# Kernel tuning notes

Measured on AMD Instinct MI355X. Metric: run time of the kernel, lower is better.

The kernel has to match this reference:

```python
import jax, jax.numpy as jnp
import numpy as np


def setup_inputs() -> dict:
    key = jax.random.key(0)
    ks = jax.random.split(key, 13)
    B, D, H, O = 4096, 2048, 3, 1  # batch, input_dim, hidden layer count, output_dim
    f32 = jnp.float32
    scale = 1.0 / np.sqrt(D)
    return {
        "x": jax.random.normal(ks[0], (B, D), f32),
        "w_mu_h": jax.random.normal(ks[1], (H, D, D), f32) * scale,
        "w_rho_h": jax.random.normal(ks[2], (H, D, D), f32) - 5.0,  # softplus(-5) ~ small std
        "b_mu_h": jax.random.normal(ks[3], (H, D), f32) * scale,
        "b_rho_h": jax.random.normal(ks[4], (H, D), f32) - 5.0,
        "w_mu_o": jax.random.normal(ks[5], (O, D), f32) * scale,
        "w_rho_o": jax.random.normal(ks[6], (O, D), f32) - 5.0,
        "b_mu_o": jax.random.normal(ks[7], (O,), f32) * scale,
        "b_rho_o": jax.random.normal(ks[8], (O,), f32) - 5.0,
        # reparameterization noise (torch.randn_like), passed explicitly for determinism
        "eps_w_h": jax.random.normal(ks[9], (H, D, D), f32),
        "eps_b_h": jax.random.normal(ks[10], (H, D), f32),
        "eps_w_o": jax.random.normal(ks[11], (O, D), f32),
        "eps_b_o": jax.random.normal(ks[12], (O,), f32),
    }


def _vlinear(x, w_mu, w_rho, b_mu, b_rho, eps_w, eps_b):
    # weight = mu + eps * softplus(rho); F.linear(x, W, b) = x @ W.T + b
    w = w_mu + eps_w * jax.nn.softplus(w_rho)
    b = b_mu + eps_b * jax.nn.softplus(b_rho)
    return x @ w.T + b


def reference(x, w_mu_h, w_rho_h, b_mu_h, b_rho_h,
              w_mu_o, w_rho_o, b_mu_o, b_rho_o,
              eps_w_h, eps_b_h, eps_w_o, eps_b_o):
    def step(h, p):
        wm, wr, bm, br, ew, eb = p
        h = jax.nn.relu(_vlinear(h, wm, wr, bm, br, ew, eb))
        return h, None

    h, _ = jax.lax.scan(step, x, (w_mu_h, w_rho_h, b_mu_h, b_rho_h, eps_w_h, eps_b_h))
    return _vlinear(h, w_mu_o, w_rho_o, b_mu_o, b_rho_o, eps_w_o, eps_b_o)
```

## Files before the change

### kernel.cpp

```cpp
#include <hip/hip_runtime.h>

#define BB 4096
#define DD 2048

typedef float f32x4 __attribute__((ext_vector_type(4)));
typedef __bf16 bf16x8 __attribute__((ext_vector_type(8)));

typedef __attribute__((address_space(1))) unsigned int gl_u32;
typedef __attribute__((address_space(3))) unsigned int lds_u32;

#define GLOAD_LDS16(gptr, sptr) \
  __builtin_amdgcn_global_load_lds((gl_u32*)(void*)(gptr), (lds_u32*)(sptr), 16, 0, 0)

#define SBAR_MEM() asm volatile("s_barrier" ::: "memory")
#define VMCNT(n)   asm volatile("s_waitcnt vmcnt(" #n ")" ::: "memory")

__device__ __forceinline__ unsigned short f2bf(float f) {
  unsigned int u = __float_as_uint(f);
  u += 0x7fffu + ((u >> 16) & 1u);
  return (unsigned short)(u >> 16);
}

__device__ __forceinline__ float sp(float x) {
  float t = __expf(-fabsf(x));
  return fmaxf(x, 0.0f) + __logf(1.0f + t);
}

__device__ __forceinline__ void prep_w_vec4(
    const float* __restrict__ mu, const float* __restrict__ rho,
    const float* __restrict__ eps, unsigned short* __restrict__ Wh,
    long long i)
{
  float4 m = ((const float4*)mu)[i];
  float4 r = ((const float4*)rho)[i];
  float4 e = ((const float4*)eps)[i];
  ushort4 o;
  o.x = f2bf(m.x + e.x * sp(r.x));
  o.y = f2bf(m.y + e.y * sp(r.y));
  o.z = f2bf(m.z + e.z * sp(r.z));
  o.w = f2bf(m.w + e.w * sp(r.w));
  ((ushort4*)Wh)[i] = o;
}

__device__ __forceinline__ void prep_f32_vec4(
    const float* __restrict__ mu, const float* __restrict__ rho,
    const float* __restrict__ eps, float* __restrict__ out, long long i)
{
  float4 m = ((const float4*)mu)[i];
  float4 r = ((const float4*)rho)[i];
  float4 e = ((const float4*)eps)[i];
  float4 o;
  o.x = m.x + e.x * sp(r.x);
  o.y = m.y + e.y * sp(r.y);
  o.z = m.z + e.z * sp(r.z);
  o.w = m.w + e.w * sp(r.w);
  ((float4*)out)[i] = o;
}

__global__ __launch_bounds__(512) void prep0_kernel(
    const float* __restrict__ x,
    const float* __restrict__ wmuh, const float* __restrict__ wrhoh,
    const float* __restrict__ bmuh, const float* __restrict__ brhoh,
    const float* __restrict__ epswh, const float* __restrict__ epsbh,
    unsigned short* __restrict__ Wh, unsigned short* __restrict__ Xb,
    float* __restrict__ bh)
{
  const int b = blockIdx.x;
  const int t = threadIdx.x;
  if (b < 512) {
    long long base = (long long)b * 2048 + t;
    #pragma unroll
    for (int j = 0; j < 4; ++j)
      prep_w_vec4(wmuh, wrhoh, epswh, Wh, base + j * 512);
    return;
  }
  if (b < 1536) {
    long long base = (long long)(b - 512) * 2048 + t;
    #pragma unroll
    for (int j = 0; j < 4; ++j) {
      float4 v = ((const float4*)x)[base + j * 512];
      ushort4 o;
      o.x = f2bf(v.x); o.y = f2bf(v.y); o.z = f2bf(v.z); o.w = f2bf(v.w);
      ((ushort4*)Xb)[base + j * 512] = o;
    }
    return;
  }
  prep_f32_vec4(bmuh, brhoh, epsbh, bh, t);
}

#define NGEMM 256
#define ATILE 16384
#define BUFE  24576

struct Coords256 { int m0, n0; int srow[4], sgc[4]; };

__device__ __forceinline__ Coords256 coords256(int id, int t) {
  Coords256 g;
  const int p = id & 7;
  const int i4 = id >> 3;
  const int mt = (p & 3) * 4 + (i4 & 3);
  const int nt = (p >> 2) * 8 + (i4 >> 2);
  g.m0 = mt * 256;
  g.n0 = nt * 128;
  #pragma unroll
  for (int i = 0; i < 4; ++i) {
    int c = i * 512 + t;
    g.srow[i] = c >> 3;
    g.sgc[i] = (c & 7) ^ (g.srow[i] & 7);
  }
  return g;
}

__device__ __forceinline__ void stage_tile(
    const unsigned short* __restrict__ A, const unsigned short* __restrict__ W,
    unsigned short* buf, const Coords256& gc, int kt, int t)
{
  #pragma unroll
  for (int i = 0; i < 4; ++i) {
    int c = i * 512 + t;
    const unsigned short* ga = A + (size_t)(gc.m0 + gc.srow[i]) * DD + kt + gc.sgc[i] * 8;
    GLOAD_LDS16(ga, &buf[c * 8]);
  }
  #pragma unroll
  for (int i = 0; i < 2; ++i) {
    int c = i * 512 + t;
    const unsigned short* gb = W + (size_t)(gc.n0 + gc.srow[i]) * DD + kt + gc.sgc[i] * 8;
    GLOAD_LDS16(gb, &buf[ATILE + c * 8]);
  }
}

__device__ __forceinline__ void compute_ktile(
    const unsigned short* buf, int wm, int wn, int lq, int lr,
    f32x4 (&acc)[4][4])
{
  #pragma unroll
  for (int s = 0; s < 2; ++s) {
    bf16x8 af[4], bfv[4];
    const int g = s * 4 + lq;
    const int go = (g ^ (lr & 7)) * 8;
    #pragma unroll
    for (int i = 0; i < 4; ++i) {
      int ra = wm * 64 + i * 16 + lr;
      af[i] = *(const bf16x8*)&buf[ra * 64 + go];
    }
    #pragma unroll
    for (int j = 0; j < 4; ++j) {
      int rb = wn * 64 + j * 16 + lr;
      bfv[j] = *(const bf16x8*)&buf[ATILE + rb * 64 + go];
    }
    __builtin_amdgcn_s_setprio(1);
    #pragma unroll
    for (int i = 0; i < 4; ++i)
      #pragma unroll
      for (int j = 0; j < 4; ++j)
        acc[i][j] = __builtin_amdgcn_mfma_f32_16x16x32_bf16(af[i], bfv[j], acc[i][j], 0, 0, 0);
    __builtin_amdgcn_s_setprio(0);
  }
}

__device__ __forceinline__ void gemm_mainloop256(
    const unsigned short* __restrict__ A, const unsigned short* __restrict__ W,
    unsigned short (*lds)[BUFE], const Coords256& gc, int t, f32x4 (&acc)[4][4])
{
  const int l = t & 63, lq = l >> 4, lr = l & 15;
  const int w = t >> 6, wm = w & 3, wn = w >> 2;
  unsigned short *p0 = lds[0], *p1 = lds[1], *p2 = lds[2];
  stage_tile(A, W, p0, gc, 0, t);
  stage_tile(A, W, p1, gc, 64, t);
  for (int k = 0; k < 32; ++k) {
    if (k < 30) {
      stage_tile(A, W, p2, gc, (k + 2) * 64, t);
      VMCNT(12);
    } else if (k == 30) {
      VMCNT(6);
    } else {
      VMCNT(0);
    }
    SBAR_MEM();
    compute_ktile(p0, wm, wn, lq, lr, acc);
    SBAR_MEM();
    unsigned short* tmp = p0; p0 = p1; p1 = p2; p2 = tmp;
  }
}

__device__ __forceinline__ void epilogue_store256(
    const Coords256& gc, int t, f32x4 (&acc)[4][4],
    const float* __restrict__ bias, unsigned short* __restrict__ C)
{
  const int l = t & 63, lq = l >> 4, lr = l & 15;
  const int w = t >> 6, wm = w & 3, wn = w >> 2;
  #pragma unroll
  for (int j = 0; j < 4; ++j) {
    int n = gc.n0 + wn * 64 + j * 16 + lr;
    float bv = bias[n];
    #pragma unroll
    for (int i = 0; i < 4; ++i) {
      int mbase = gc.m0 + wm * 64 + i * 16 + lq * 4;
      #pragma unroll
      for (int r = 0; r < 4; ++r) {
        float v = fmaxf(acc[i][j][r] + bv, 0.0f);
        C[(size_t)(mbase + r) * DD + n] = f2bf(v);
      }
    }
  }
}

__global__ __launch_bounds__(512, 2) void gemm_relu_fused_kernel(
    const unsigned short* __restrict__ A,
    const unsigned short* __restrict__ W,
    const float* __restrict__ bias,
    unsigned short* __restrict__ C,
    const float* __restrict__ wmuh, const float* __restrict__ wrhoh,
    const float* __restrict__ bmuh, const float* __restrict__ brhoh,
    const float* __restrict__ wmuo, const float* __restrict__ wrhoo,
    const float* __restrict__ epswh, const float* __restrict__ epsbh,
    const float* __restrict__ epswo,
    unsigned short* __restrict__ Wh, float* __restrict__ bh,
    float* __restrict__ wo)
{
  __shared__ unsigned short lds[3][BUFE];

  const int id = blockIdx.x;
  const int t = threadIdx.x;

  if (id >= NGEMM) {
    const int pb = id - NGEMM;
    if (pb < 1024) {
      long long base = 1048576LL + (long long)pb * 2048 + t;
      #pragma unroll
      for (int j = 0; j < 4; ++j)
        prep_w_vec4(wmuh, wrhoh, epswh, Wh, base + j * 512);
      return;
    }
    #pragma unroll
    for (int j = 0; j < 2; ++j)
      prep_f32_vec4(bmuh, brhoh, epsbh, bh, 512 + j * 512 + t);
    prep_f32_vec4(wmuo, wrhoo, epswo, wo, t);
    return;
  }

  Coords256 gc = coords256(id, t);
  f32x4 acc[4][4] = {};
  gemm_mainloop256(A, W, lds, gc, t, acc);
  epilogue_store256(gc, t, acc, bias, C);
}

__global__ __launch_bounds__(512, 2) void gemm_relu_kernel(
    const unsigned short* __restrict__ A,
    const unsigned short* __restrict__ W,
    const float* __restrict__ bias,
    unsigned short* __restrict__ C)
{
  __shared__ unsigned short lds[3][BUFE];
  const int t = threadIdx.x;
  Coords256 gc = coords256(blockIdx.x, t);
  f32x4 acc[4][4] = {};
  gemm_mainloop256(A, W, lds, gc, t, acc);
  epilogue_store256(gc, t, acc, bias, C);
}

__global__ __launch_bounds__(512, 2) void gemm_relu_dot_kernel(
    const unsigned short* __restrict__ A,
    const unsigned short* __restrict__ W,
    const float* __restrict__ bias,
    const float* __restrict__ wo,
    float* __restrict__ Pbuf)
{
  __shared__ unsigned short lds[3][BUFE];
  const int t = threadIdx.x;

  Coords256 gc = coords256(blockIdx.x, t);
  f32x4 acc[4][4] = {};
  gemm_mainloop256(A, W, lds, gc, t, acc);

  const int l = t & 63, lq = l >> 4, lr = l & 15;
  const int w = t >> 6, wm = w & 3, wn = w >> 2;

  float bv[4], wv[4];
  #pragma unroll
  for (int j = 0; j < 4; ++j) {
    int n = gc.n0 + wn * 64 + j * 16 + lr;
    bv[j] = bias[n];
    wv[j] = wo[n];
  }
  float partial[4][4];
  #pragma unroll
  for (int i = 0; i < 4; ++i)
    #pragma unroll
    for (int r = 0; r < 4; ++r) {
      float s = 0.0f;
      #pragma unroll
      for (int j = 0; j < 4; ++j)
        s += fmaxf(acc[i][j][r] + bv[j], 0.0f) * wv[j];
      partial[i][r] = s;
    }

  #pragma unroll
  for (int d = 1; d <= 8; d <<= 1)
    #pragma unroll
    for (int i = 0; i < 4; ++i)
      #pragma unroll
      for (int r = 0; r < 4; ++r)
        partial[i][r] += __shfl_xor(partial[i][r], d, 64);

  float* sRed = (float*)lds;
  if (lr == 0) {
    #pragma unroll
    for (int i = 0; i < 4; ++i)
      #pragma unroll
      for (int r = 0; r < 4; ++r) {
        int row = wm * 64 + i * 16 + lq * 4 + r;
        sRed[row * 2 + wn] = partial[i][r];
      }
  }
  __syncthreads();
  if (t < 256) {
    float s = sRed[t * 2 + 0] + sRed[t * 2 + 1];
    int nt = gc.n0 >> 7;
    Pbuf[nt * BB + gc.m0 + t] = s;
  }
}

__global__ __launch_bounds__(256) void reduce_out_kernel(
    const float* __restrict__ Pbuf,
    const float* __restrict__ bmuo, const float* __restrict__ brhoo,
    const float* __restrict__ epsbo,
    float* __restrict__ out)
{
  const int m = blockIdx.x * 256 + threadIdx.x;
  float s = bmuo[0] + epsbo[0] * sp(brhoo[0]);
  #pragma unroll
  for (int nt = 0; nt < 16; ++nt)
    s += Pbuf[nt * BB + m];
  out[m] = s;
}

extern "C" void kernel_launch(void* const* d_in, const int* in_sizes, int n_in,
                              void* d_out, int out_size, void* d_ws, size_t ws_size,
                              hipStream_t stream) {
  const float* x     = (const float*)d_in[0];
  const float* wmuh  = (const float*)d_in[1];
  const float* wrhoh = (const float*)d_in[2];
  const float* bmuh  = (const float*)d_in[3];
  const float* brhoh = (const float*)d_in[4];
  const float* wmuo  = (const float*)d_in[5];
  const float* wrhoo = (const float*)d_in[6];
  const float* bmuo  = (const float*)d_in[7];
  const float* brhoo = (const float*)d_in[8];
  const float* epswh = (const float*)d_in[9];
  const float* epsbh = (const float*)d_in[10];
  const float* epswo = (const float*)d_in[11];
  const float* epsbo = (const float*)d_in[12];

  char* ws = (char*)d_ws;
  unsigned short* Wh = (unsigned short*)(ws);
  unsigned short* Xb = (unsigned short*)(ws + 25165824);
  unsigned short* Ha = (unsigned short*)(ws + 25165824 + 16777216);
  unsigned short* Hb = (unsigned short*)(ws + 25165824 + 2 * 16777216);
  float* bh   = (float*)(ws + 25165824 + 3 * 16777216);
  float* wo   = (float*)(ws + 25165824 + 3 * 16777216 + 24576);
  float* Pbuf = (float*)(ws + 25165824 + 3 * 16777216 + 24576 + 8192);

  prep0_kernel<<<1537, 512, 0, stream>>>(
      x, wmuh, wrhoh, bmuh, brhoh, epswh, epsbh, Wh, Xb, bh);

  gemm_relu_fused_kernel<<<NGEMM + 1025, 512, 0, stream>>>(
      Xb, Wh, bh, Ha,
      wmuh, wrhoh, bmuh, brhoh, wmuo, wrhoo,
      epswh, epsbh, epswo, Wh, bh, wo);

  gemm_relu_kernel<<<NGEMM, 512, 0, stream>>>(Ha, Wh + 1 * 4194304, bh + DD, Hb);

  gemm_relu_dot_kernel<<<NGEMM, 512, 0, stream>>>(
      Hb, Wh + 2 * 4194304, bh + 2 * DD, wo, Pbuf);

  reduce_out_kernel<<<BB / 256, 256, 0, stream>>>(
      Pbuf, bmuo, brhoo, epsbo, (float*)d_out);
}
```

Baseline: 320.4 us.

## Split k-tile staging into halves and move all weight prep into prep kernel

The GEMM main loop now issues each k-tile's global-to-LDS loads in two halves interleaved with the two MFMA sub-steps. It also adds an explicit lgkmcnt wait and sched_barriers, with the aim of overlapping memory traffic with compute more finely. The first GEMM no longer runs hidden-layer weight preparation in extra blocks alongside it; all weight, bias and output-weight prep moves into the single prep kernel. This removes co-scheduling of elementwise work with the first GEMM but serializes the prep before any GEMM starts.

```diff
diff --git a/kernel.cpp b/kernel.cpp
--- a/kernel.cpp
+++ b/kernel.cpp
@@ -14,6 +14,7 @@
 
 #define SBAR_MEM() asm volatile("s_barrier" ::: "memory")
 #define VMCNT(n)   asm volatile("s_waitcnt vmcnt(" #n ")" ::: "memory")
+#define LGKMCNT0() asm volatile("s_waitcnt lgkmcnt(0)" ::: "memory")
 
 __device__ __forceinline__ unsigned short f2bf(float f) {
   unsigned int u = __float_as_uint(f);
@@ -61,21 +62,23 @@
     const float* __restrict__ x,
     const float* __restrict__ wmuh, const float* __restrict__ wrhoh,
     const float* __restrict__ bmuh, const float* __restrict__ brhoh,
+    const float* __restrict__ wmuo, const float* __restrict__ wrhoo,
     const float* __restrict__ epswh, const float* __restrict__ epsbh,
+    const float* __restrict__ epswo,
     unsigned short* __restrict__ Wh, unsigned short* __restrict__ Xb,
-    float* __restrict__ bh)
+    float* __restrict__ bh, float* __restrict__ wo)
 {
   const int b = blockIdx.x;
   const int t = threadIdx.x;
-  if (b < 512) {
+  if (b < 1536) {
     long long base = (long long)b * 2048 + t;
     #pragma unroll
     for (int j = 0; j < 4; ++j)
       prep_w_vec4(wmuh, wrhoh, epswh, Wh, base + j * 512);
     return;
   }
-  if (b < 1536) {
-    long long base = (long long)(b - 512) * 2048 + t;
+  if (b < 2560) {
+    long long base = (long long)(b - 1536) * 2048 + t;
     #pragma unroll
     for (int j = 0; j < 4; ++j) {
       float4 v = ((const float4*)x)[base + j * 512];
@@ -85,12 +88,13 @@
     }
     return;
   }
-  prep_f32_vec4(bmuh, brhoh, epsbh, bh, t);
+  #pragma unroll
+  for (int j = 0; j < 3; ++j)
+    prep_f32_vec4(bmuh, brhoh, epsbh, bh, j * 512 + t);
+  prep_f32_vec4(wmuo, wrhoo, epswo, wo, t);
 }
 
 #define NGEMM 256
-#define ATILE 16384
-#define BUFE  24576
 
 struct Coords256 { int m0, n0; int srow[4], sgc[4]; };
 
@@ -111,75 +115,91 @@
   return g;
 }
 
-__device__ __forceinline__ void stage_tile(
+__device__ __forceinline__ void stage_half0(
     const unsigned short* __restrict__ A, const unsigned short* __restrict__ W,
-    unsigned short* buf, const Coords256& gc, int kt, int t)
-{
-  #pragma unroll
-  for (int i = 0; i < 4; ++i) {
+    unsigned short* bufA, unsigned short* bufB,
+    const Coords256& gc, int kt, int t)
+{
+  #pragma unroll
+  for (int i = 0; i < 2; ++i) {
     int c = i * 512 + t;
     const unsigned short* ga = A + (size_t)(gc.m0 + gc.srow[i]) * DD + kt + gc.sgc[i] * 8;
-    GLOAD_LDS16(ga, &buf[c * 8]);
-  }
-  #pragma unroll
-  for (int i = 0; i < 2; ++i) {
+    GLOAD_LDS16(ga, &bufA[c * 8]);
+  }
+  const unsigned short* gb = W + (size_t)(gc.n0 + gc.srow[0]) * DD + kt + gc.sgc[0] * 8;
+  GLOAD_LDS16(gb, &bufB[t * 8]);
+}
+
+__device__ __forceinline__ void stage_half1(
+    const unsigned short* __restrict__ A, const unsigned short* __restrict__ W,
+    unsigned short* bufA, unsigned short* bufB,
+    const Coords256& gc, int kt, int t)
+{
+  #pragma unroll
+  for (int i = 2; i < 4; ++i) {
     int c = i * 512 + t;
-    const unsigned short* gb = W + (size_t)(gc.n0 + gc.srow[i]) * DD + kt + gc.sgc[i] * 8;
-    GLOAD_LDS16(gb, &buf[ATILE + c * 8]);
-  }
-}
-
-__device__ __forceinline__ void compute_ktile(
-    const unsigned short* buf, int wm, int wn, int lq, int lr,
-    f32x4 (&acc)[4][4])
-{
-  #pragma unroll
-  for (int s = 0; s < 2; ++s) {
-    bf16x8 af[4], bfv[4];
-    const int g = s * 4 + lq;
-    const int go = (g ^ (lr & 7)) * 8;
-    #pragma unroll
-    for (int i = 0; i < 4; ++i) {
-      int ra = wm * 64 + i * 16 + lr;
-      af[i] = *(const bf16x8*)&buf[ra * 64 + go];
-    }
-    #pragma unroll
-    for (int j = 0; j < 4; ++j) {
-      int rb = wn * 64 + j * 16 + lr;
-      bfv[j] = *(const bf16x8*)&buf[ATILE + rb * 64 + go];
-    }
-    __builtin_amdgcn_s_setprio(1);
-    #pragma unroll
-    for (int i = 0; i < 4; ++i)
-      #pragma unroll
-      for (int j = 0; j < 4; ++j)
-        acc[i][j] = __builtin_amdgcn_mfma_f32_16x16x32_bf16(af[i], bfv[j], acc[i][j], 0, 0, 0);
-    __builtin_amdgcn_s_setprio(0);
-  }
-}
-
-__device__ __forceinline__ void gemm_mainloop256(
+    const unsigned short* ga = A + (size_t)(gc.m0 + gc.srow[i]) * DD + kt + gc.sgc[i] * 8;
+    GLOAD_LDS16(ga, &bufA[c * 8]);
+  }
+  const unsigned short* gb = W + (size_t)(gc.n0 + gc.srow[1]) * DD + kt + gc.sgc[1] * 8;
+  GLOAD_LDS16(gb, &bufB[(512 + t) * 8]);
+}
+
+__device__ __forceinline__ void compute_half(
+    const unsigned short* bufA, const unsigned short* bufB, int s,
+    int wm, int wn, int lq, int lr, f32x4 (&acc)[4][4])
+{
+  bf16x8 af[4], bfv[4];
+  const int g = s * 4 + lq;
+  const int go = (g ^ (lr & 7)) * 8;
+  #pragma unroll
+  for (int i = 0; i < 4; ++i) {
+    int ra = wm * 64 + i * 16 + lr;
+    af[i] = *(const bf16x8*)&bufA[ra * 64 + go];
+  }
+  #pragma unroll
+  for (int j = 0; j < 4; ++j) {
+    int rb = wn * 64 + j * 16 + lr;
+    bfv[j] = *(const bf16x8*)&bufB[rb * 64 + go];
+  }
+  LGKMCNT0();
+  __builtin_amdgcn_sched_barrier(0);
+  __builtin_amdgcn_s_setprio(1);
+  #pragma unroll
+  for (int i = 0; i < 4; ++i)
+    #pragma unroll
+    for (int j = 0; j < 4; ++j)
+      acc[i][j] = __builtin_amdgcn_mfma_f32_16x16x32_bf16(af[i], bfv[j], acc[i][j], 0, 0, 0);
+  __builtin_amdgcn_s_setprio(0);
+}
+
+__device__ __forceinline__ void gemm_mainloop8p(
     const unsigned short* __restrict__ A, const unsigned short* __restrict__ W,
-    unsigned short (*lds)[BUFE], const Coords256& gc, int t, f32x4 (&acc)[4][4])
+    unsigned short (*ldsA)[16384], unsigned short (*ldsB)[8192],
+    const Coords256& gc, int t, f32x4 (&acc)[4][4])
 {
   const int l = t & 63, lq = l >> 4, lr = l & 15;
   const int w = t >> 6, wm = w & 3, wn = w >> 2;
-  unsigned short *p0 = lds[0], *p1 = lds[1], *p2 = lds[2];
-  stage_tile(A, W, p0, gc, 0, t);
-  stage_tile(A, W, p1, gc, 64, t);
+  unsigned short *a0 = ldsA[0], *a1 = ldsA[1], *a2 = ldsA[2];
+  unsigned short *b0 = ldsB[0], *b1 = ldsB[1], *b2 = ldsB[2];
+  stage_half0(A, W, a0, b0, gc, 0, t);
+  stage_half1(A, W, a0, b0, gc, 0, t);
+  stage_half0(A, W, a1, b1, gc, 64, t);
+  stage_half1(A, W, a1, b1, gc, 64, t);
   for (int k = 0; k < 32; ++k) {
-    if (k < 30) {
-      stage_tile(A, W, p2, gc, (k + 2) * 64, t);
-      VMCNT(12);
-    } else if (k == 30) {
-      VMCNT(6);
-    } else {
-      VMCNT(0);
-    }
+    if (k < 30) stage_half0(A, W, a2, b2, gc, (k + 2) * 64, t);
+    __builtin_amdgcn_sched_barrier(0);
+    if (k < 30)      { VMCNT(9); }
+    else if (k == 30){ VMCNT(6); }
+    else             { VMCNT(0); }
     SBAR_MEM();
-    compute_ktile(p0, wm, wn, lq, lr, acc);
+    compute_half(a0, b0, 0, wm, wn, lq, lr, acc);
     SBAR_MEM();
-    unsigned short* tmp = p0; p0 = p1; p1 = p2; p2 = tmp;
+    if (k < 30) stage_half1(A, W, a2, b2, gc, (k + 2) * 64, t);
+    compute_half(a0, b0, 1, wm, wn, lq, lr, acc);
+    SBAR_MEM();
+    unsigned short* ta = a0; a0 = a1; a1 = a2; a2 = ta;
+    unsigned short* tb = b0; b0 = b1; b1 = b2; b2 = tb;
   }
 }
 
@@ -205,57 +225,18 @@
   }
 }
 
-__global__ __launch_bounds__(512, 2) void gemm_relu_fused_kernel(
-    const unsigned short* __restrict__ A,
-    const unsigned short* __restrict__ W,
-    const float* __restrict__ bias,
-    unsigned short* __restrict__ C,
-    const float* __restrict__ wmuh, const float* __restrict__ wrhoh,
-    const float* __restrict__ bmuh, const float* __restrict__ brhoh,
-    const float* __restrict__ wmuo, const float* __restrict__ wrhoo,
-    const float* __restrict__ epswh, const float* __restrict__ epsbh,
-    const float* __restrict__ epswo,
-    unsigned short* __restrict__ Wh, float* __restrict__ bh,
-    float* __restrict__ wo)
-{
-  __shared__ unsigned short lds[3][BUFE];
-
-  const int id = blockIdx.x;
-  const int t = threadIdx.x;
-
-  if (id >= NGEMM) {
-    const int pb = id - NGEMM;
-    if (pb < 1024) {
-      long long base = 1048576LL + (long long)pb * 2048 + t;
-      #pragma unroll
-      for (int j = 0; j < 4; ++j)
-        prep_w_vec4(wmuh, wrhoh, epswh, Wh, base + j * 512);
-      return;
-    }
-    #pragma unroll
-    for (int j = 0; j < 2; ++j)
-      prep_f32_vec4(bmuh, brhoh, epsbh, bh, 512 + j * 512 + t);
-    prep_f32_vec4(wmuo, wrhoo, epswo, wo, t);
-    return;
-  }
-
-  Coords256 gc = coords256(id, t);
-  f32x4 acc[4][4] = {};
-  gemm_mainloop256(A, W, lds, gc, t, acc);
-  epilogue_store256(gc, t, acc, bias, C);
-}
-
 __global__ __launch_bounds__(512, 2) void gemm_relu_kernel(
     const unsigned short* __restrict__ A,
     const unsigned short* __restrict__ W,
     const float* __restrict__ bias,
     unsigned short* __restrict__ C)
 {
-  __shared__ unsigned short lds[3][BUFE];
+  __shared__ unsigned short ldsA[3][16384];
+  __shared__ unsigned short ldsB[3][8192];
   const int t = threadIdx.x;
   Coords256 gc = coords256(blockIdx.x, t);
   f32x4 acc[4][4] = {};
-  gemm_mainloop256(A, W, lds, gc, t, acc);
+  gemm_mainloop8p(A, W, ldsA, ldsB, gc, t, acc);
   epilogue_store256(gc, t, acc, bias, C);
 }
 
@@ -266,12 +247,13 @@
     const float* __restrict__ wo,
     float* __restrict__ Pbuf)
 {
-  __shared__ unsigned short lds[3][BUFE];
+  __shared__ unsigned short ldsA[3][16384];
+  __shared__ unsigned short ldsB[3][8192];
   const int t = threadIdx.x;
 
   Coords256 gc = coords256(blockIdx.x, t);
   f32x4 acc[4][4] = {};
-  gemm_mainloop256(A, W, lds, gc, t, acc);
+  gemm_mainloop8p(A, W, ldsA, ldsB, gc, t, acc);
 
   const int l = t & 63, lq = l >> 4, lr = l & 15;
   const int w = t >> 6, wm = w & 3, wn = w >> 2;
@@ -303,7 +285,7 @@
       for (int r = 0; r < 4; ++r)
         partial[i][r] += __shfl_xor(partial[i][r], d, 64);
 
-  float* sRed = (float*)lds;
+  float* sRed = (float*)ldsA;
   if (lr == 0) {
     #pragma unroll
     for (int i = 0; i < 4; ++i)
@@ -361,13 +343,11 @@
   float* wo   = (float*)(ws + 25165824 + 3 * 16777216 + 24576);
   float* Pbuf = (float*)(ws + 25165824 + 3 * 16777216 + 24576 + 8192);
 
-  prep0_kernel<<<1537, 512, 0, stream>>>(
-      x, wmuh, wrhoh, bmuh, brhoh, epswh, epsbh, Wh, Xb, bh);
-
-  gemm_relu_fused_kernel<<<NGEMM + 1025, 512, 0, stream>>>(
-      Xb, Wh, bh, Ha,
-      wmuh, wrhoh, bmuh, brhoh, wmuo, wrhoo,
-      epswh, epsbh, epswo, Wh, bh, wo);
+  prep0_kernel<<<2561, 512, 0, stream>>>(
+      x, wmuh, wrhoh, bmuh, brhoh, wmuo, wrhoo,
+      epswh, epsbh, epswo, Wh, Xb, bh, wo);
+
+  gemm_relu_kernel<<<NGEMM, 512, 0, stream>>>(Xb, Wh, bh, Ha);
 
   gemm_relu_kernel<<<NGEMM, 512, 0, stream>>>(Ha, Wh + 1 * 4194304, bh + DD, Hb);
 
```

New measurement: 335.5 us. 1.05x slower.
